# Kernel optimization log

Hardware: AMD Instinct MI355X
Metric: run time of the kernel (lower is better)

## Reference

```python
import jax, jax.numpy as jnp
import numpy as np

B, T, H = 4, 4096, 1024
E = 8                      # num_experts
K = 2                      # experts_per_token
F = 4096 // E * 2          # expert_ffn_dim = 1024
LB_COEFF = 0.01


def setup_inputs() -> dict:
    key = jax.random.key(0)
    ks = jax.random.split(key, 5)
    s = 0.02
    return {
        "x": jax.random.normal(ks[0], (B, T, H), dtype=jnp.float32),
        "router_w": jax.random.normal(ks[1], (E, H), dtype=jnp.float32) * s,   # Linear weight [out,in]
        "gate_w": jax.random.normal(ks[2], (E, F, H), dtype=jnp.float32) * s,
        "up_w": jax.random.normal(ks[3], (E, F, H), dtype=jnp.float32) * s,
        "down_w": jax.random.normal(ks[4], (E, H, F), dtype=jnp.float32) * s,
    }


def reference(x, router_w, gate_w, up_w, down_w):
    b, t, h = x.shape
    xf = x.reshape(-1, h)                              # [N,H]
    n = xf.shape[0]
    logits = xf @ router_w.T                           # [N,E]
    probs = jax.nn.softmax(logits, axis=-1)
    top_v, top_i = jax.lax.top_k(probs, K)             # [N,K]
    top_v = top_v / jnp.sum(top_v, axis=-1, keepdims=True)
    # dense gate matrix: gates[n,e] = normalized prob if expert e in top-k of token n else 0
    gates = jnp.zeros_like(probs).at[jnp.arange(n)[:, None], top_i].set(top_v)  # [N,E]
    out = jnp.zeros_like(xf)
    for e in range(E):  # small fixed expert loop; SwiGLU FFN per expert, gated combine
        hid = jax.nn.silu(xf @ gate_w[e].T) * (xf @ up_w[e].T)   # [N,F]
        out = out + gates[:, e:e + 1] * (hid @ down_w[e].T)      # weighted scatter-add
    out = out.reshape(b, t, h)
    usage = probs.mean(axis=0)                          # [E]
    lb_loss = LB_COEFF * (E * jnp.sum(usage * usage))
    return out, lb_loss
```

## Files before the change

kernel.cpp:

```cpp
#include <hip/hip_runtime.h>
#include <math.h>

#define N_TOK 16384
#define HD    1024
#define FD    1024
#define NE    8
#define NA    (N_TOK * 2)
#define MBLK  128
#define MAX_MB 264

typedef __attribute__((ext_vector_type(8))) short bf16x8;
typedef __attribute__((ext_vector_type(4))) short bf16x4;
typedef __attribute__((ext_vector_type(4))) float f32x4;

#define WS_USAGE  0u
#define WS_COUNTS 64u
#define WS_OFFS   128u
#define WS_CURSOR 192u
#define WS_TBLN   256u
#define WS_BLKE   320u
#define WS_BLKM   (WS_BLKE + 1088u)
#define WS_TOKE   8192u
#define WS_TOKG   (WS_TOKE + NA * 4u)
#define WS_TOKP   (WS_TOKG + NA * 4u)
#define WS_ATOK   (WS_TOKP + NA * 4u)
#define WS_AGATE  (WS_ATOK + NA * 4u)
#define WS_XB     (1u << 20)
#define WS_GWB    (WS_XB  + 33554432u)
#define WS_UWB    (WS_GWB + 16777216u)
#define WS_DWB    (WS_UWB + 16777216u)
#define WS_HID    (WS_DWB + 16777216u)
#define WS_Y      WS_XB

__device__ __forceinline__ short f2b(float f) {
    union { float f; unsigned u; } c;
    c.f = f;
    unsigned u = (c.u + 0x7fffu + ((c.u >> 16) & 1u)) >> 16;
    return (short)u;
}
__device__ __forceinline__ float b2f(short s) {
    union { unsigned u; float f; } c;
    c.u = ((unsigned)(unsigned short)s) << 16;
    return c.f;
}

__device__ __forceinline__ void gl_lds16(const short* g, short* l) {
    __builtin_amdgcn_global_load_lds(
        (const __attribute__((address_space(1))) unsigned int*)g,
        (__attribute__((address_space(3))) unsigned int*)l,
        16, 0, 0);
}

__global__ __launch_bounds__(256) void cvt3_kernel(
    const float* __restrict__ gw, const float* __restrict__ uw, const float* __restrict__ dw,
    short* __restrict__ gwb, short* __restrict__ uwb, short* __restrict__ dwb,
    int* __restrict__ ws_counters) {
    if (blockIdx.x == 0 && blockIdx.y == 0 && threadIdx.x < 64)
        ws_counters[threadIdx.x] = 0;
    const float* in  = (blockIdx.y == 0) ? gw  : (blockIdx.y == 1) ? uw  : dw;
    short*       out = (blockIdx.y == 0) ? gwb : (blockIdx.y == 1) ? uwb : dwb;
    const int i = blockIdx.x * 256 + threadIdx.x;
    const float4 a = ((const float4*)in)[2 * i];
    const float4 b = ((const float4*)in)[2 * i + 1];
    bf16x8 o;
    o[0] = f2b(a.x); o[1] = f2b(a.y); o[2] = f2b(a.z); o[3] = f2b(a.w);
    o[4] = f2b(b.x); o[5] = f2b(b.y); o[6] = f2b(b.z); o[7] = f2b(b.w);
    ((bf16x8*)out)[i] = o;
}

__global__ __launch_bounds__(512) void router_kernel(
    const float* __restrict__ x, const float* __restrict__ rw,
    float* __restrict__ usage, int* __restrict__ counts,
    int* __restrict__ tok_e, float* __restrict__ tok_g, short* __restrict__ xb)
{
    __shared__ float rws[NE * HD];
    __shared__ float usage_s[NE];
    __shared__ int counts_s[NE];
    const int tid = threadIdx.x;
    if (tid < NE) { usage_s[tid] = 0.f; counts_s[tid] = 0; }
    for (int c = tid; c < NE * HD / 4; c += 512)
        ((float4*)rws)[c] = ((const float4*)rw)[c];
    __syncthreads();

    const int wave = tid >> 6, lane = tid & 63;
    const int t = blockIdx.x * 8 + wave;
    float acc[NE];
#pragma unroll
    for (int e = 0; e < NE; ++e) acc[e] = 0.f;
    const float* xrow = x + (size_t)t * HD;
    short* xbrow = xb + (size_t)t * HD;
#pragma unroll
    for (int j = 0; j < 4; ++j) {
        const int h0 = (j * 64 + lane) * 4;
        const float4 xv = *(const float4*)(xrow + h0);
        bf16x4 xc;
        xc[0] = f2b(xv.x); xc[1] = f2b(xv.y); xc[2] = f2b(xv.z); xc[3] = f2b(xv.w);
        *(bf16x4*)(xbrow + h0) = xc;
#pragma unroll
        for (int e = 0; e < NE; ++e) {
            const float4 wv = *(const float4*)&rws[e * HD + h0];
            acc[e] += xv.x * wv.x + xv.y * wv.y + xv.z * wv.z + xv.w * wv.w;
        }
    }
#pragma unroll
    for (int e = 0; e < NE; ++e)
#pragma unroll
        for (int off = 32; off > 0; off >>= 1)
            acc[e] += __shfl_xor(acc[e], off, 64);

    if (lane == 0) {
        float mx = acc[0];
        for (int e = 1; e < NE; ++e) mx = fmaxf(mx, acc[e]);
        float p[NE], Z = 0.f;
        for (int e = 0; e < NE; ++e) { p[e] = expf(acc[e] - mx); Z += p[e]; }
        const float invZ = 1.f / Z;
        for (int e = 0; e < NE; ++e) { p[e] *= invZ; atomicAdd(&usage_s[e], p[e]); }
        int i0 = 0;
        for (int e = 1; e < NE; ++e) if (acc[e] > acc[i0]) i0 = e;
        int i1 = (i0 == 0) ? 1 : 0;
        for (int e = 0; e < NE; ++e) if (e != i0 && acc[e] > acc[i1]) i1 = e;
        const float gs = 1.f / (p[i0] + p[i1]);
        tok_e[2 * t] = i0;  tok_e[2 * t + 1] = i1;
        tok_g[2 * t] = p[i0] * gs;  tok_g[2 * t + 1] = p[i1] * gs;
        atomicAdd(&counts_s[i0], 1); atomicAdd(&counts_s[i1], 1);
    }
    __syncthreads();
    if (tid < NE) {
        atomicAdd(&usage[tid], usage_s[tid]);
        atomicAdd(&counts[tid], counts_s[tid]);
    }
}

__global__ void offsets_lb_kernel(const float* __restrict__ usage,
                                  const int* __restrict__ counts,
                                  int* __restrict__ offs, float* __restrict__ lb_out,
                                  int* __restrict__ tbl_n, int* __restrict__ blk_e,
                                  int* __restrict__ blk_m)
{
    if (threadIdx.x == 0) {
        int acc = 0, nb = 0;
        for (int e = 0; e < NE; ++e) {
            offs[e] = acc;
            const int c = counts[e];
            acc += c;
            for (int mb = 0; mb < c; mb += MBLK) { blk_e[nb] = e; blk_m[nb] = mb; ++nb; }
        }
        offs[NE] = acc;
        tbl_n[0] = nb;
        float s = 0.f;
        for (int e = 0; e < NE; ++e) {
            const float u = usage[e] * (1.f / (float)N_TOK);
            s += u * u;
        }
        lb_out[0] = 0.01f * 8.f * s;
    }
}

__global__ __launch_bounds__(256) void scatter_kernel(
    const int* __restrict__ tok_e, const float* __restrict__ tok_g,
    const int* __restrict__ offs, int* __restrict__ cursor,
    int* __restrict__ asg_tok, float* __restrict__ asg_g,
    int* __restrict__ tok_pos)
{
    __shared__ int cnt_s[NE];
    __shared__ int base_s[NE];
    const int tid = threadIdx.x;
    if (tid < NE) cnt_s[tid] = 0;
    __syncthreads();

    const int idx = blockIdx.x * 256 + tid;
    const int e = tok_e[idx];
    const int local = atomicAdd(&cnt_s[e], 1);
    __syncthreads();

    if (tid < NE) base_s[tid] = atomicAdd(&cursor[tid], cnt_s[tid]);
    __syncthreads();

    const int pos = offs[e] + base_s[e] + local;
    asg_tok[pos] = idx >> 1;
    asg_g[pos] = tok_g[idx];
    tok_pos[idx] = pos;
}


__global__ __launch_bounds__(256, 4) void gemm1_kernel(
    const short* __restrict__ xb, const short* __restrict__ gate_b,
    const short* __restrict__ up_b, const int* __restrict__ counts,
    const int* __restrict__ offs, const int* __restrict__ asg_tok,
    const int* __restrict__ tbl_n, const int* __restrict__ blk_e,
    const int* __restrict__ blk_m, short* __restrict__ hid)
{
    __shared__ short As[128 * 64];
    __shared__ short Bg[64 * 64];
    __shared__ short Bu[64 * 64];

    const int wg  = blockIdx.x;
    const int swz = (wg & 7) * (16 * MAX_MB / 8) + (wg >> 3);
    const int m_id = swz >> 4;
    const int n_base = (swz & 15) * 64;
    if (m_id >= tbl_n[0]) return;
    const int e = blk_e[m_id];
    const int m_base = blk_m[m_id];
    const int n_e = counts[e];
    const int off_e = offs[e];

    const int tid = threadIdx.x;
    const int wave = tid >> 6, lane = tid & 63;
    const int lr = lane >> 3, lg = lane & 7;
    const int sg = lg ^ lr;

    const short* a_src[4];
#pragma unroll
    for (int j = 0; j < 4; ++j) {
        const int r = wave * 32 + j * 8 + lr;
        const int gm = m_base + r;
        const int tok = asg_tok[off_e + (gm < n_e ? gm : 0)];
        a_src[j] = xb + (size_t)tok * HD + sg * 8;
    }
    const short* gwp = gate_b + (size_t)e * FD * HD;
    const short* uwp = up_b + (size_t)e * FD * HD;
    const short* bg_src[2]; const short* bu_src[2];
#pragma unroll
    for (int j = 0; j < 2; ++j) {
        const int r = wave * 16 + j * 8 + lr;
        bg_src[j] = gwp + (size_t)(n_base + r) * HD + sg * 8;
        bu_src[j] = uwp + (size_t)(n_base + r) * HD + sg * 8;
    }

    const int wm = (wave >> 1) * 64;
    const int wn = (wave & 1) * 32;
    const int quad = lane >> 4, l16 = lane & 15;

    f32x4 accG[4][2], accU[4][2];
#pragma unroll
    for (int mi = 0; mi < 4; ++mi)
#pragma unroll
        for (int ni = 0; ni < 2; ++ni) { accG[mi][ni] = (f32x4){0,0,0,0}; accU[mi][ni] = (f32x4){0,0,0,0}; }

    for (int t = 0; t < 16; ++t) {
        const int k0 = t * 64;
#pragma unroll
        for (int j = 0; j < 4; ++j)
            gl_lds16(a_src[j] + k0, &As[(wave * 32 + j * 8) * 64]);
#pragma unroll
        for (int j = 0; j < 2; ++j) {
            gl_lds16(bg_src[j] + k0, &Bg[(wave * 16 + j * 8) * 64]);
            gl_lds16(bu_src[j] + k0, &Bu[(wave * 16 + j * 8) * 64]);
        }
        __syncthreads();
#pragma unroll
        for (int kk8 = 0; kk8 < 8; kk8 += 4) {
            bf16x8 a[4];
#pragma unroll
            for (int mi = 0; mi < 4; ++mi) {
                const int row = wm + mi * 16 + l16;
                const int pg = (kk8 + quad) ^ (row & 7);
                a[mi] = *(const bf16x8*)&As[row * 64 + pg * 8];
            }
#pragma unroll
            for (int ni = 0; ni < 2; ++ni) {
                const int row = wn + ni * 16 + l16;
                const int pg = (kk8 + quad) ^ (row & 7);
                bf16x8 bg = *(const bf16x8*)&Bg[row * 64 + pg * 8];
                bf16x8 bu = *(const bf16x8*)&Bu[row * 64 + pg * 8];
#pragma unroll
                for (int mi = 0; mi < 4; ++mi) {
                    accG[mi][ni] = __builtin_amdgcn_mfma_f32_16x16x32_bf16(a[mi], bg, accG[mi][ni], 0, 0, 0);
                    accU[mi][ni] = __builtin_amdgcn_mfma_f32_16x16x32_bf16(a[mi], bu, accU[mi][ni], 0, 0, 0);
                }
            }
        }
        __syncthreads();
    }

#pragma unroll
    for (int mi = 0; mi < 4; ++mi) {
#pragma unroll
        for (int r = 0; r < 4; ++r) {
            const int gm = m_base + wm + mi * 16 + quad * 4 + r;
            if (gm < n_e) {
#pragma unroll
                for (int ni = 0; ni < 2; ++ni) {
                    const int f = n_base + wn + ni * 16 + l16;
                    const float gv = accG[mi][ni][r];
                    const float uv = accU[mi][ni][r];
                    hid[(size_t)(off_e + gm) * FD + f] = f2b((gv / (1.f + expf(-gv))) * uv);
                }
            }
        }
    }
}

__global__ __launch_bounds__(256, 4) void gemm2_kernel(
    const short* __restrict__ hid, const short* __restrict__ down_b,
    const int* __restrict__ counts, const int* __restrict__ offs,
    const float* __restrict__ asg_g, const int* __restrict__ tbl_n,
    const int* __restrict__ blk_e, const int* __restrict__ blk_m,
    short* __restrict__ Y)
{
    __shared__ short As[128 * 64];
    __shared__ short Bs[128 * 64];

    const int wg  = blockIdx.x;
    const int swz = (wg & 7) * (8 * MAX_MB / 8) + (wg >> 3);
    const int m_id = swz >> 3;
    const int n_base = (swz & 7) * 128;
    if (m_id >= tbl_n[0]) return;
    const int e = blk_e[m_id];
    const int m_base = blk_m[m_id];
    const int n_e = counts[e];
    const int off_e = offs[e];

    const int tid = threadIdx.x;
    const int wave = tid >> 6, lane = tid & 63;
    const int lr = lane >> 3, lg = lane & 7;
    const int sg = lg ^ lr;

    const short* a_src[4]; const short* b_src[4];
    const short* bwp = down_b + (size_t)e * HD * FD;
#pragma unroll
    for (int j = 0; j < 4; ++j) {
        const int r = wave * 32 + j * 8 + lr;
        const int gm = m_base + r;
        const size_t srow = (size_t)(off_e + (gm < n_e ? gm : 0));
        a_src[j] = hid + srow * FD + sg * 8;
        b_src[j] = bwp + (size_t)(n_base + r) * FD + sg * 8;
    }

    const int wm = (wave >> 1) * 64;
    const int wn = (wave & 1) * 64;
    const int quad = lane >> 4, l16 = lane & 15;

    f32x4 acc[4][4];
#pragma unroll
    for (int mi = 0; mi < 4; ++mi)
#pragma unroll
        for (int ni = 0; ni < 4; ++ni) acc[mi][ni] = (f32x4){0,0,0,0};

    for (int t = 0; t < 16; ++t) {
        const int k0 = t * 64;
#pragma unroll
        for (int j = 0; j < 4; ++j) {
            gl_lds16(a_src[j] + k0, &As[(wave * 32 + j * 8) * 64]);
            gl_lds16(b_src[j] + k0, &Bs[(wave * 32 + j * 8) * 64]);
        }
        __syncthreads();
#pragma unroll
        for (int kk8 = 0; kk8 < 8; kk8 += 4) {
            bf16x8 a[4], b[4];
#pragma unroll
            for (int mi = 0; mi < 4; ++mi) {
                const int row = wm + mi * 16 + l16;
                const int pg = (kk8 + quad) ^ (row & 7);
                a[mi] = *(const bf16x8*)&As[row * 64 + pg * 8];
            }
#pragma unroll
            for (int ni = 0; ni < 4; ++ni) {
                const int row = wn + ni * 16 + l16;
                const int pg = (kk8 + quad) ^ (row & 7);
                b[ni] = *(const bf16x8*)&Bs[row * 64 + pg * 8];
            }
#pragma unroll
            for (int mi = 0; mi < 4; ++mi)
#pragma unroll
                for (int ni = 0; ni < 4; ++ni)
                    acc[mi][ni] = __builtin_amdgcn_mfma_f32_16x16x32_bf16(a[mi], b[ni], acc[mi][ni], 0, 0, 0);
        }
        __syncthreads();
    }

#pragma unroll
    for (int mi = 0; mi < 4; ++mi) {
#pragma unroll
        for (int r = 0; r < 4; ++r) {
            const int gm = m_base + wm + mi * 16 + quad * 4 + r;
            if (gm < n_e) {
                const int pos = off_e + gm;
                const float gate = asg_g[pos];
                short* yrow = Y + (size_t)pos * HD;
#pragma unroll
                for (int ni = 0; ni < 4; ++ni) {
                    const int n = n_base + wn + ni * 16 + l16;
                    yrow[n] = f2b(acc[mi][ni][r] * gate);
                }
            }
        }
    }
}

__global__ __launch_bounds__(256) void combine_kernel(
    const short* __restrict__ Y, const int* __restrict__ tok_pos, float* __restrict__ out)
{
    const int g = blockIdx.x * 256 + threadIdx.x;
    const int t  = g >> 7;
    const int w8 = (g & 127) * 8;
    const int p0 = tok_pos[2 * t], p1 = tok_pos[2 * t + 1];
    const bf16x8 y0 = *(const bf16x8*)(Y + (size_t)p0 * HD + w8);
    const bf16x8 y1 = *(const bf16x8*)(Y + (size_t)p1 * HD + w8);
    float4 o0, o1;
    o0.x = b2f(y0[0]) + b2f(y1[0]); o0.y = b2f(y0[1]) + b2f(y1[1]);
    o0.z = b2f(y0[2]) + b2f(y1[2]); o0.w = b2f(y0[3]) + b2f(y1[3]);
    o1.x = b2f(y0[4]) + b2f(y1[4]); o1.y = b2f(y0[5]) + b2f(y1[5]);
    o1.z = b2f(y0[6]) + b2f(y1[6]); o1.w = b2f(y0[7]) + b2f(y1[7]);
    float* orow = out + (size_t)t * HD + w8;
    *(float4*)orow = o0;
    *(float4*)(orow + 4) = o1;
}

extern "C" void kernel_launch(void* const* d_in, const int* in_sizes, int n_in,
                              void* d_out, int out_size, void* d_ws, size_t ws_size,
                              hipStream_t stream)
{
    const float* x  = (const float*)d_in[0];
    const float* rw = (const float*)d_in[1];
    const float* gw = (const float*)d_in[2];
    const float* uw = (const float*)d_in[3];
    const float* dw = (const float*)d_in[4];
    float* out = (float*)d_out;

    char* ws = (char*)d_ws;
    float* usage = (float*)(ws + WS_USAGE);
    int* counts  = (int*)(ws + WS_COUNTS);
    int* offs    = (int*)(ws + WS_OFFS);
    int* cursor  = (int*)(ws + WS_CURSOR);
    int* tbl_n   = (int*)(ws + WS_TBLN);
    int* blk_e   = (int*)(ws + WS_BLKE);
    int* blk_m   = (int*)(ws + WS_BLKM);
    int* tok_e   = (int*)(ws + WS_TOKE);
    float* tok_g = (float*)(ws + WS_TOKG);
    int* tok_pos = (int*)(ws + WS_TOKP);
    int* asg_tok = (int*)(ws + WS_ATOK);
    float* asg_g = (float*)(ws + WS_AGATE);
    short* xb    = (short*)(ws + WS_XB);
    short* gwb   = (short*)(ws + WS_GWB);
    short* uwb   = (short*)(ws + WS_UWB);
    short* dwb   = (short*)(ws + WS_DWB);
    short* hid   = (short*)(ws + WS_HID);
    short* Y     = (short*)(ws + WS_Y);

    cvt3_kernel<<<dim3((NE * FD * HD / 8) / 256, 3), 256, 0, stream>>>(
        gw, uw, dw, gwb, uwb, dwb, (int*)ws);
    router_kernel<<<N_TOK / 8, 512, 0, stream>>>(x, rw, usage, counts, tok_e, tok_g, xb);
    offsets_lb_kernel<<<1, 64, 0, stream>>>(usage, counts, offs, out + 16777216,
                                            tbl_n, blk_e, blk_m);
    scatter_kernel<<<NA / 256, 256, 0, stream>>>(tok_e, tok_g, offs, cursor,
                                                 asg_tok, asg_g, tok_pos);
    gemm1_kernel<<<16 * MAX_MB, 256, 0, stream>>>(
        xb, gwb, uwb, counts, offs, asg_tok, tbl_n, blk_e, blk_m, hid);
    gemm2_kernel<<<8 * MAX_MB, 256, 0, stream>>>(
        hid, dwb, counts, offs, asg_g, tbl_n, blk_e, blk_m, Y);
    combine_kernel<<<(N_TOK * HD / 8) / 256, 256, 0, stream>>>(Y, tok_pos, out);
}
```

Baseline: 464.2 us.

## Merge weight conversion into router, drop offsets kernel, compute partitions inline

Folds the bf16 weight-conversion blocks into the router launch as extra blocks, replaces the in-kernel counter clear with a memset, and removes the single-thread offsets/block-table kernel. GEMM kernels now derive their expert, row base and offset on the fly from the per-expert counts. The scatter kernel computes prefix offsets and the load-balance loss itself. The GEMM inner loops also precompute the swizzled LDS offsets outside the k-loop. The aim is fewer launches and serial gaps, at the cost of a small per-block lookup loop and one extra memset call.

```diff
diff --git a/kernel.cpp b/kernel.cpp
--- a/kernel.cpp
+++ b/kernel.cpp
@@ -15,11 +15,7 @@
 
 #define WS_USAGE  0u
 #define WS_COUNTS 64u
-#define WS_OFFS   128u
 #define WS_CURSOR 192u
-#define WS_TBLN   256u
-#define WS_BLKE   320u
-#define WS_BLKM   (WS_BLKE + 1088u)
 #define WS_TOKE   8192u
 #define WS_TOKG   (WS_TOKE + NA * 4u)
 #define WS_TOKP   (WS_TOKG + NA * 4u)
@@ -51,25 +47,29 @@
         16, 0, 0);
 }
 
-__global__ __launch_bounds__(256) void cvt3_kernel(
+__device__ __forceinline__ int partition_lookup(
+    const int* __restrict__ counts, int m_id,
+    int* e_out, int* m_base, int* off_e, int* n_e)
+{
+    int off = 0, rem = m_id, found = 0, e = 0, cnt = 0;
+#pragma unroll
+    for (int ee = 0; ee < NE; ++ee) {
+        const int c = counts[ee];
+        const int nb = (c + MBLK - 1) >> 7;
+        if (!found) {
+            if (rem >= nb) { rem -= nb; off += c; }
+            else { e = ee; cnt = c; found = 1; }
+        }
+    }
+    *e_out = e; *m_base = rem * MBLK; *off_e = off; *n_e = cnt;
+    return found;
+}
+
+#define RTR_BLKS 2048
+__global__ __launch_bounds__(512) void cvt_router_kernel(
+    const float* __restrict__ x, const float* __restrict__ rw,
     const float* __restrict__ gw, const float* __restrict__ uw, const float* __restrict__ dw,
     short* __restrict__ gwb, short* __restrict__ uwb, short* __restrict__ dwb,
-    int* __restrict__ ws_counters) {
-    if (blockIdx.x == 0 && blockIdx.y == 0 && threadIdx.x < 64)
-        ws_counters[threadIdx.x] = 0;
-    const float* in  = (blockIdx.y == 0) ? gw  : (blockIdx.y == 1) ? uw  : dw;
-    short*       out = (blockIdx.y == 0) ? gwb : (blockIdx.y == 1) ? uwb : dwb;
-    const int i = blockIdx.x * 256 + threadIdx.x;
-    const float4 a = ((const float4*)in)[2 * i];
-    const float4 b = ((const float4*)in)[2 * i + 1];
-    bf16x8 o;
-    o[0] = f2b(a.x); o[1] = f2b(a.y); o[2] = f2b(a.z); o[3] = f2b(a.w);
-    o[4] = f2b(b.x); o[5] = f2b(b.y); o[6] = f2b(b.z); o[7] = f2b(b.w);
-    ((bf16x8*)out)[i] = o;
-}
-
-__global__ __launch_bounds__(512) void router_kernel(
-    const float* __restrict__ x, const float* __restrict__ rw,
     float* __restrict__ usage, int* __restrict__ counts,
     int* __restrict__ tok_e, float* __restrict__ tok_g, short* __restrict__ xb)
 {
@@ -77,13 +77,30 @@
     __shared__ float usage_s[NE];
     __shared__ int counts_s[NE];
     const int tid = threadIdx.x;
+    const int blk = blockIdx.x;
+
+    if (blk >= RTR_BLKS) {
+        const int cb = blk - RTR_BLKS;
+        const int tensor = cb >> 11;
+        const float* in  = (tensor == 0) ? gw  : (tensor == 1) ? uw  : dw;
+        short*       out = (tensor == 0) ? gwb : (tensor == 1) ? uwb : dwb;
+        const int i = (cb & 2047) * 512 + tid;
+        const float4 a = ((const float4*)in)[2 * i];
+        const float4 b = ((const float4*)in)[2 * i + 1];
+        bf16x8 o;
+        o[0] = f2b(a.x); o[1] = f2b(a.y); o[2] = f2b(a.z); o[3] = f2b(a.w);
+        o[4] = f2b(b.x); o[5] = f2b(b.y); o[6] = f2b(b.z); o[7] = f2b(b.w);
+        ((bf16x8*)out)[i] = o;
+        return;
+    }
+
     if (tid < NE) { usage_s[tid] = 0.f; counts_s[tid] = 0; }
     for (int c = tid; c < NE * HD / 4; c += 512)
         ((float4*)rws)[c] = ((const float4*)rw)[c];
     __syncthreads();
 
     const int wave = tid >> 6, lane = tid & 63;
-    const int t = blockIdx.x * 8 + wave;
+    const int t = blk * 8 + wave;
     float acc[NE];
 #pragma unroll
     for (int e = 0; e < NE; ++e) acc[e] = 0.f;
@@ -131,36 +148,12 @@
     }
 }
 
-__global__ void offsets_lb_kernel(const float* __restrict__ usage,
-                                  const int* __restrict__ counts,
-                                  int* __restrict__ offs, float* __restrict__ lb_out,
-                                  int* __restrict__ tbl_n, int* __restrict__ blk_e,
-                                  int* __restrict__ blk_m)
-{
-    if (threadIdx.x == 0) {
-        int acc = 0, nb = 0;
-        for (int e = 0; e < NE; ++e) {
-            offs[e] = acc;
-            const int c = counts[e];
-            acc += c;
-            for (int mb = 0; mb < c; mb += MBLK) { blk_e[nb] = e; blk_m[nb] = mb; ++nb; }
-        }
-        offs[NE] = acc;
-        tbl_n[0] = nb;
-        float s = 0.f;
-        for (int e = 0; e < NE; ++e) {
-            const float u = usage[e] * (1.f / (float)N_TOK);
-            s += u * u;
-        }
-        lb_out[0] = 0.01f * 8.f * s;
-    }
-}
-
 __global__ __launch_bounds__(256) void scatter_kernel(
     const int* __restrict__ tok_e, const float* __restrict__ tok_g,
-    const int* __restrict__ offs, int* __restrict__ cursor,
+    const int* __restrict__ counts, const float* __restrict__ usage,
+    int* __restrict__ cursor,
     int* __restrict__ asg_tok, float* __restrict__ asg_g,
-    int* __restrict__ tok_pos)
+    int* __restrict__ tok_pos, float* __restrict__ lb_out)
 {
     __shared__ int cnt_s[NE];
     __shared__ int base_s[NE];
@@ -176,19 +169,31 @@
     if (tid < NE) base_s[tid] = atomicAdd(&cursor[tid], cnt_s[tid]);
     __syncthreads();
 
-    const int pos = offs[e] + base_s[e] + local;
+    int offs_e = 0;
+#pragma unroll
+    for (int ee = 0; ee < NE; ++ee) if (ee < e) offs_e += counts[ee];
+
+    const int pos = offs_e + base_s[e] + local;
     asg_tok[pos] = idx >> 1;
     asg_g[pos] = tok_g[idx];
     tok_pos[idx] = pos;
+
+    if (blockIdx.x == 0 && tid == 0) {
+        float s = 0.f;
+#pragma unroll
+        for (int ee = 0; ee < NE; ++ee) {
+            const float u = usage[ee] * (1.f / (float)N_TOK);
+            s += u * u;
+        }
+        lb_out[0] = 0.01f * 8.f * s;
+    }
 }
 
 
 __global__ __launch_bounds__(256, 4) void gemm1_kernel(
     const short* __restrict__ xb, const short* __restrict__ gate_b,
     const short* __restrict__ up_b, const int* __restrict__ counts,
-    const int* __restrict__ offs, const int* __restrict__ asg_tok,
-    const int* __restrict__ tbl_n, const int* __restrict__ blk_e,
-    const int* __restrict__ blk_m, short* __restrict__ hid)
+    const int* __restrict__ asg_tok, short* __restrict__ hid)
 {
     __shared__ short As[128 * 64];
     __shared__ short Bg[64 * 64];
@@ -198,11 +203,9 @@
     const int swz = (wg & 7) * (16 * MAX_MB / 8) + (wg >> 3);
     const int m_id = swz >> 4;
     const int n_base = (swz & 15) * 64;
-    if (m_id >= tbl_n[0]) return;
-    const int e = blk_e[m_id];
-    const int m_base = blk_m[m_id];
-    const int n_e = counts[e];
-    const int off_e = offs[e];
+
+    int e, m_base, off_e, n_e;
+    if (!partition_lookup(counts, m_id, &e, &m_base, &off_e, &n_e)) return;
 
     const int tid = threadIdx.x;
     const int wave = tid >> 6, lane = tid & 63;
@@ -231,6 +234,21 @@
     const int wn = (wave & 1) * 32;
     const int quad = lane >> 4, l16 = lane & 15;
 
+    int aoff[2][4], boff[2][2];
+#pragma unroll
+    for (int s = 0; s < 2; ++s) {
+#pragma unroll
+        for (int mi = 0; mi < 4; ++mi) {
+            const int row = wm + mi * 16 + l16;
+            aoff[s][mi] = row * 64 + (((s * 4 + quad) ^ (row & 7)) * 8);
+        }
+#pragma unroll
+        for (int ni = 0; ni < 2; ++ni) {
+            const int row = wn + ni * 16 + l16;
+            boff[s][ni] = row * 64 + (((s * 4 + quad) ^ (row & 7)) * 8);
+        }
+    }
+
     f32x4 accG[4][2], accU[4][2];
 #pragma unroll
     for (int mi = 0; mi < 4; ++mi)
@@ -249,20 +267,15 @@
         }
         __syncthreads();
 #pragma unroll
-        for (int kk8 = 0; kk8 < 8; kk8 += 4) {
+        for (int s = 0; s < 2; ++s) {
             bf16x8 a[4];
 #pragma unroll
-            for (int mi = 0; mi < 4; ++mi) {
-                const int row = wm + mi * 16 + l16;
-                const int pg = (kk8 + quad) ^ (row & 7);
-                a[mi] = *(const bf16x8*)&As[row * 64 + pg * 8];
-            }
+            for (int mi = 0; mi < 4; ++mi)
+                a[mi] = *(const bf16x8*)&As[aoff[s][mi]];
 #pragma unroll
             for (int ni = 0; ni < 2; ++ni) {
-                const int row = wn + ni * 16 + l16;
-                const int pg = (kk8 + quad) ^ (row & 7);
-                bf16x8 bg = *(const bf16x8*)&Bg[row * 64 + pg * 8];
-                bf16x8 bu = *(const bf16x8*)&Bu[row * 64 + pg * 8];
+                const bf16x8 bg = *(const bf16x8*)&Bg[boff[s][ni]];
+                const bf16x8 bu = *(const bf16x8*)&Bu[boff[s][ni]];
 #pragma unroll
                 for (int mi = 0; mi < 4; ++mi) {
                     accG[mi][ni] = __builtin_amdgcn_mfma_f32_16x16x32_bf16(a[mi], bg, accG[mi][ni], 0, 0, 0);
@@ -293,9 +306,7 @@
 
 __global__ __launch_bounds__(256, 4) void gemm2_kernel(
     const short* __restrict__ hid, const short* __restrict__ down_b,
-    const int* __restrict__ counts, const int* __restrict__ offs,
-    const float* __restrict__ asg_g, const int* __restrict__ tbl_n,
-    const int* __restrict__ blk_e, const int* __restrict__ blk_m,
+    const int* __restrict__ counts, const float* __restrict__ asg_g,
     short* __restrict__ Y)
 {
     __shared__ short As[128 * 64];
@@ -305,11 +316,9 @@
     const int swz = (wg & 7) * (8 * MAX_MB / 8) + (wg >> 3);
     const int m_id = swz >> 3;
     const int n_base = (swz & 7) * 128;
-    if (m_id >= tbl_n[0]) return;
-    const int e = blk_e[m_id];
-    const int m_base = blk_m[m_id];
-    const int n_e = counts[e];
-    const int off_e = offs[e];
+
+    int e, m_base, off_e, n_e;
+    if (!partition_lookup(counts, m_id, &e, &m_base, &off_e, &n_e)) return;
 
     const int tid = threadIdx.x;
     const int wave = tid >> 6, lane = tid & 63;
@@ -331,6 +340,21 @@
     const int wn = (wave & 1) * 64;
     const int quad = lane >> 4, l16 = lane & 15;
 
+    int aoff[2][4], boff[2][4];
+#pragma unroll
+    for (int s = 0; s < 2; ++s) {
+#pragma unroll
+        for (int mi = 0; mi < 4; ++mi) {
+            const int row = wm + mi * 16 + l16;
+            aoff[s][mi] = row * 64 + (((s * 4 + quad) ^ (row & 7)) * 8);
+        }
+#pragma unroll
+        for (int ni = 0; ni < 4; ++ni) {
+            const int row = wn + ni * 16 + l16;
+            boff[s][ni] = row * 64 + (((s * 4 + quad) ^ (row & 7)) * 8);
+        }
+    }
+
     f32x4 acc[4][4];
 #pragma unroll
     for (int mi = 0; mi < 4; ++mi)
@@ -346,20 +370,14 @@
         }
         __syncthreads();
 #pragma unroll
-        for (int kk8 = 0; kk8 < 8; kk8 += 4) {
+        for (int s = 0; s < 2; ++s) {
             bf16x8 a[4], b[4];
 #pragma unroll
-            for (int mi = 0; mi < 4; ++mi) {
-                const int row = wm + mi * 16 + l16;
-                const int pg = (kk8 + quad) ^ (row & 7);
-                a[mi] = *(const bf16x8*)&As[row * 64 + pg * 8];
-            }
-#pragma unroll
-            for (int ni = 0; ni < 4; ++ni) {
-                const int row = wn + ni * 16 + l16;
-                const int pg = (kk8 + quad) ^ (row & 7);
-                b[ni] = *(const bf16x8*)&Bs[row * 64 + pg * 8];
-            }
+            for (int mi = 0; mi < 4; ++mi)
+                a[mi] = *(const bf16x8*)&As[aoff[s][mi]];
+#pragma unroll
+            for (int ni = 0; ni < 4; ++ni)
+                b[ni] = *(const bf16x8*)&Bs[boff[s][ni]];
 #pragma unroll
             for (int mi = 0; mi < 4; ++mi)
 #pragma unroll
@@ -421,11 +439,7 @@
     char* ws = (char*)d_ws;
     float* usage = (float*)(ws + WS_USAGE);
     int* counts  = (int*)(ws + WS_COUNTS);
-    int* offs    = (int*)(ws + WS_OFFS);
     int* cursor  = (int*)(ws + WS_CURSOR);
-    int* tbl_n   = (int*)(ws + WS_TBLN);
-    int* blk_e   = (int*)(ws + WS_BLKE);
-    int* blk_m   = (int*)(ws + WS_BLKM);
     int* tok_e   = (int*)(ws + WS_TOKE);
     float* tok_g = (float*)(ws + WS_TOKG);
     int* tok_pos = (int*)(ws + WS_TOKP);
@@ -438,16 +452,14 @@
     short* hid   = (short*)(ws + WS_HID);
     short* Y     = (short*)(ws + WS_Y);
 
-    cvt3_kernel<<<dim3((NE * FD * HD / 8) / 256, 3), 256, 0, stream>>>(
-        gw, uw, dw, gwb, uwb, dwb, (int*)ws);
-    router_kernel<<<N_TOK / 8, 512, 0, stream>>>(x, rw, usage, counts, tok_e, tok_g, xb);
-    offsets_lb_kernel<<<1, 64, 0, stream>>>(usage, counts, offs, out + 16777216,
-                                            tbl_n, blk_e, blk_m);
-    scatter_kernel<<<NA / 256, 256, 0, stream>>>(tok_e, tok_g, offs, cursor,
-                                                 asg_tok, asg_g, tok_pos);
+    hipMemsetAsync(d_ws, 0, 256, stream);
+    cvt_router_kernel<<<RTR_BLKS + 3 * 2048, 512, 0, stream>>>(
+        x, rw, gw, uw, dw, gwb, uwb, dwb, usage, counts, tok_e, tok_g, xb);
+    scatter_kernel<<<NA / 256, 256, 0, stream>>>(
+        tok_e, tok_g, counts, usage, cursor, asg_tok, asg_g, tok_pos, out + 16777216);
     gemm1_kernel<<<16 * MAX_MB, 256, 0, stream>>>(
-        xb, gwb, uwb, counts, offs, asg_tok, tbl_n, blk_e, blk_m, hid);
+        xb, gwb, uwb, counts, asg_tok, hid);
     gemm2_kernel<<<8 * MAX_MB, 256, 0, stream>>>(
-        hid, dwb, counts, offs, asg_g, tbl_n, blk_e, blk_m, Y);
+        hid, dwb, counts, asg_g, Y);
     combine_kernel<<<(N_TOK * HD / 8) / 256, 256, 0, stream>>>(Y, tok_pos, out);
 }
```

Result: faster. 451.9 us (-2.6%).
